# Kernel optimization log

Hardware: AMD Instinct MI355X
Metric: run time of the kernel (lower is better)

The kernel has to match this reference:

```python
import jax, jax.numpy as jnp
import numpy as np

B, N, C = 4, 4096, 16
HID, HEADS, OUT = 64, 4, 64
NEG = -1e16

def setup_inputs() -> dict:
    key = jax.random.key(0)
    ks = jax.random.split(key, 7)
    x = jax.random.normal(ks[0], (B, N, C), dtype=jnp.float32)
    # sparse-ish binary adjacency with self-loops, stored dense as in the torch module
    graph = (jax.random.randint(ks[1], (N, N), 0, 2)).astype(jnp.float32)
    graph = jnp.maximum(graph, jnp.eye(N, dtype=jnp.float32))
    # per-head Linear weights (bias=False) and the per-layer bias parameter b
    Ws = jax.random.normal(ks[2], (HEADS, C, HID), dtype=jnp.float32)   # W.weight.T per head
    bs = jax.random.normal(ks[3], (HEADS, HID), dtype=jnp.float32)
    W_out = jax.random.normal(ks[4], (HEADS * HID, OUT), dtype=jnp.float32)
    b_out = jax.random.normal(ks[5], (OUT,), dtype=jnp.float32)
    return {"x": x, "graph": graph, "Ws": Ws, "bs": bs, "W_out": W_out, "b_out": b_out}

def _gat_layer(x, graph, W, b):
    # x: [B,N,Cin], W: [Cin,D], b: [D]
    h = jnp.einsum('bnc,cd->bnd', x, W)                      # [B,N,D]
    s = jnp.einsum('bnd,bmd->bnm', h, h) * graph[None]       # [B,N,N]
    s = jnp.where(s == 0.0, NEG, s)                          # masked_fill(eq 0, -1e16)
    attn = jax.nn.softmax(s, axis=2)
    return jnp.einsum('bnm,bmd->bnd', attn, h) + b

def _leaky_relu(x):
    return jnp.where(x >= 0, x, 0.2 * x)

def reference(x, graph, Ws, bs, W_out, b_out):
    # multi-head layers, concatenated on feature dim (head-major)
    heads = jax.vmap(lambda W, b: _gat_layer(x, graph, W, b))(Ws, bs)  # [H,B,N,D]
    cat = jnp.transpose(heads, (1, 2, 0, 3)).reshape(B, N, HEADS * HID)
    cat = _leaky_relu(cat)
    out = _gat_layer(cat, graph, W_out, b_out)
    return _leaky_relu(out)
```

## Files before the change

### kernel.cpp

```cpp
#include <hip/hip_runtime.h>

typedef unsigned short u16;
typedef unsigned int u32;
typedef unsigned long long u64;
typedef __attribute__((ext_vector_type(8))) short bf16x8;
typedef __attribute__((ext_vector_type(4))) float f32x4;
typedef __attribute__((ext_vector_type(16))) float f32x16;

#define NEGF  -1.0e38f
#define MINIT -1.0e30f
#define LOG2E 1.4426950408889634f

__device__ __forceinline__ u16 f2bf(float x) {
  union { float f; u32 u; } v; v.f = x;
  u32 r = v.u + 0x7fffu + ((v.u >> 16) & 1u);
  return (u16)(r >> 16);
}
__device__ __forceinline__ float bf2f(u16 b) {
  union { u32 u; float f; } v; v.u = ((u32)b) << 16;
  return v.f;
}
__device__ __forceinline__ float bcast(u32 u) {
  union { u32 u; float f; } v; v.u = u; return v.f;
}
__device__ __forceinline__ u32 cvtpk(float a, float b) {
  u32 r;
  asm("v_cvt_pk_bf16_f32 %0, %1, %2" : "=v"(r) : "v"(a), "v"(b));
  return r;
}
__device__ __forceinline__ float vexp2(float x) {
  float r;
  asm("v_exp_f32 %0, %1" : "=v"(r) : "v"(x));
  return r;
}
__device__ __forceinline__ float fmax3(float a, float b, float c) {
  return fmaxf(fmaxf(a, b), c);
}
__device__ __forceinline__ float leaky(float x) { return x >= 0.f ? x : 0.2f * x; }

__device__ __forceinline__ void gload16(const void* g, void* l) {
  __builtin_amdgcn_global_load_lds(
      (const __attribute__((address_space(1))) u32*)(unsigned long long)g,
      (__attribute__((address_space(3))) u32*)(u32)(unsigned long long)l,
      16, 0, 0);
}

#define GRP   1040
#define TILE  8320
#define KA_OFF 0
#define KB_OFF 8320
#define KC_OFF 16640
#define V_OFF  24960
#define SMEM_BYTES 58240

__global__ __launch_bounds__(256) void pack_kernel(const float* __restrict__ graph,
                                                   u64* __restrict__ bits) {
  const int n = blockIdx.x;
  const int w = threadIdx.x >> 6, lane = threadIdx.x & 63;
  const float* gr = graph + (size_t)n * 4096;
  for (int j = 0; j < 16; ++j) {
    const int wd = j * 4 + w;
    u64 m = __ballot(gr[wd * 64 + lane] != 0.0f);
    if (lane == 0) bits[(size_t)wd * 4096 + n] = m;
  }
}

__global__ __launch_bounds__(256) void h1_kernel(const float* __restrict__ x,
                                                 const float* __restrict__ Ws,
                                                 u16* __restrict__ h1a, u16* __restrict__ h1b,
                                                 u16* __restrict__ h1c,
                                                 u16* __restrict__ h1aT, u16* __restrict__ h1bT) {
  const int n0 = blockIdx.x * 64;
  const int p  = blockIdx.y;
  const int b = p >> 2, h = p & 3;
  const int t = threadIdx.x;
  const int d = t & 63, rg = t >> 6;
  __shared__ float xt[64][17];
  __shared__ u16 ta[64][66];
  __shared__ u16 tb[64][66];
  {
    const float4 v = *(const float4*)(x + ((size_t)b * 4096 + n0 + (t >> 2)) * 16 + (t & 3) * 4);
    xt[t >> 2][(t & 3) * 4 + 0] = v.x;
    xt[t >> 2][(t & 3) * 4 + 1] = v.y;
    xt[t >> 2][(t & 3) * 4 + 2] = v.z;
    xt[t >> 2][(t & 3) * 4 + 3] = v.w;
  }
  float Wd[16];
  #pragma unroll
  for (int c = 0; c < 16; ++c) Wd[c] = Ws[h * (16 * 64) + c * 64 + d];
  __syncthreads();
  #pragma unroll
  for (int it = 0; it < 16; ++it) {
    const int r = it * 4 + rg;
    float acc = 0.f;
    #pragma unroll
    for (int c = 0; c < 16; ++c) acc += xt[r][c] * Wd[c];
    const size_t o = ((size_t)p * 4096 + n0 + r) * 64 + d;
    u16 a = f2bf(acc);
    float r1 = acc - bf2f(a);
    u16 bq = f2bf(r1);
    float r2 = r1 - bf2f(bq);
    h1a[o] = a; h1b[o] = bq; h1c[o] = f2bf(r2);
    ta[r][d] = a; tb[r][d] = bq;
  }
  __syncthreads();
  const int cs = (d & 51) | ((d & 4) << 1) | ((d & 8) >> 1);
  #pragma unroll
  for (int i = 0; i < 16; ++i) {
    const int dr = i * 4 + rg;
    h1aT[((size_t)p * 64 + dr) * 4096 + n0 + cs] = ta[d][dr];
    h1bT[((size_t)p * 64 + dr) * 4096 + n0 + cs] = tb[d][dr];
  }
}

__global__ __launch_bounds__(256) void transpose_kernel(const u16* __restrict__ src,
                                                        u16* __restrict__ dst) {
  const int p = blockIdx.y, n0 = blockIdx.x * 64;
  const u16* s = src + (size_t)p * 4096 * 64;
  u16* d = dst + (size_t)p * 4096 * 64;
  __shared__ u16 tile[64][66];
  const int col = threadIdx.x & 63, r4 = threadIdx.x >> 6;
  #pragma unroll
  for (int i = 0; i < 16; ++i) {
    const int r = i * 4 + r4;
    tile[r][col] = s[(size_t)(n0 + r) * 64 + col];
  }
  __syncthreads();
  const int cs = (col & 51) | ((col & 4) << 1) | ((col & 8) >> 1);
  #pragma unroll
  for (int i = 0; i < 16; ++i) {
    const int r = i * 4 + r4;
    d[(size_t)r * 4096 + n0 + cs] = tile[col][r];
  }
}

__global__ __launch_bounds__(256) void h2_kernel(const float* __restrict__ cat,
                                                 const float* __restrict__ Wout,
                                                 u16* __restrict__ h2a, u16* __restrict__ h2b,
                                                 u16* __restrict__ h2c) {
  const int row = blockIdx.x * 4 + (threadIdx.x >> 6);
  const int d = threadIdx.x & 63;
  const float* cr = cat + (size_t)row * 256;
  float acc = 0.f;
  for (int c4 = 0; c4 < 64; ++c4) {
    const float4 cv = *(const float4*)(cr + c4 * 4);
    acc += cv.x * Wout[(c4 * 4 + 0) * 64 + d];
    acc += cv.y * Wout[(c4 * 4 + 1) * 64 + d];
    acc += cv.z * Wout[(c4 * 4 + 2) * 64 + d];
    acc += cv.w * Wout[(c4 * 4 + 3) * 64 + d];
  }
  const size_t o = (size_t)row * 64 + d;
  u16 a = f2bf(acc);
  float r1 = acc - bf2f(a);
  u16 bq = f2bf(r1);
  float r2 = r1 - bf2f(bq);
  h2a[o] = a; h2b[o] = bq; h2c[o] = f2bf(r2);
}

template <int LAYER>
__global__ __launch_bounds__(256) void attn_kernel(
    const u16* __restrict__ Ha, const u16* __restrict__ Hb, const u16* __restrict__ Hc,
    const u16* __restrict__ HaT, const u16* __restrict__ HbT,
    const u64* __restrict__ bits, const float* __restrict__ bias,
    float* __restrict__ outp, float* __restrict__ pm, float* __restrict__ pl) {
  constexpr int NCH = (LAYER == 1) ? 64 : 16;
  const int orig = blockIdx.x + 32 * blockIdx.y;
  const int sid = (orig & 7) * 64 + (orig >> 3);
  const int bx = sid & 31;
  const int py = sid >> 5;
  const int pass = (LAYER == 1) ? py : (py & 3);
  const int chg0 = (LAYER == 1) ? 0 : ((py >> 2) * 16);

  const int t = threadIdx.x;
  const int wq = t >> 6;
  const int lane = t & 63;
  const int c = lane & 31;
  const int g1 = lane >> 5;
  const int qbase = bx * 128 + wq * 32;
  const int q = qbase + c;
  const size_t poffb = (size_t)pass * (4096 * 64) * 2;

  __shared__ f32x4 smem_v[SMEM_BYTES / 16];
  char* smem = (char*)smem_v;

  const int srow = lane >> 3;
  const int scol = ((lane & 7) ^ srow) << 4;
  const char* gKa = (const char*)Ha + poffb;
  const char* gKb = (const char*)Hb + poffb;
  const char* gKc = (const char*)Hc + poffb;
  const char* gVa = (const char*)HaT + poffb;
  const char* gVb = (const char*)HbT + poffb;

  auto stageK = [&](int chg) {
    const size_t cb = (size_t)chg * 8192;
    #pragma unroll
    for (int ii = 0; ii < 2; ++ii) {
      const int g = wq * 2 + ii;
      const size_t so = cb + (size_t)(g * 8 + srow) * 128 + scol;
      const int dofs = g * GRP;
      gload16(gKa + so, smem + KA_OFF + dofs);
      gload16(gKb + so, smem + KB_OFF + dofs);
      gload16(gKc + so, smem + KC_OFF + dofs);
    }
  };
  auto stageV = [&](int chg, int buf) {
    const char* gsrc = (wq >> 1) ? gVb : gVa;
    char* dbase = smem + V_OFF + buf * 16640 + (wq >> 1) * TILE;
    const size_t cb = (size_t)chg * 128;
    #pragma unroll
    for (int ii = 0; ii < 4; ++ii) {
      const int g = (wq & 1) * 4 + ii;
      const size_t so = cb + (size_t)(g * 8 + srow) * 8192 + scol;
      gload16(gsrc + so, dbase + g * GRP);
    }
  };

  bf16x8 qf[3][4];
  {
    const char* qra = (const char*)Ha + poffb + (size_t)q * 128 + 16 * g1;
    const char* qrb = (const char*)Hb + poffb + (size_t)q * 128 + 16 * g1;
    const char* qrc = (const char*)Hc + poffb + (size_t)q * 128 + 16 * g1;
    #pragma unroll
    for (int kk = 0; kk < 4; ++kk) {
      qf[0][kk] = *(const bf16x8*)(qra + kk * 32);
      qf[1][kk] = *(const bf16x8*)(qrb + kk * 32);
      qf[2][kk] = *(const bf16x8*)(qrc + kk * 32);
    }
  }

  const u64* bqp = bits + q;

  const int swz = (c & 7) << 4;
  int iK[4];
  #pragma unroll
  for (int kk = 0; kk < 4; ++kk)
    iK[kk] = c * 128 + ((c >> 3) << 4) + ((32 * kk + 16 * g1) ^ swz);

  const f32x16 z16 = {};
  f32x16 Of0, Of1;
  #pragma unroll
  for (int r = 0; r < 16; ++r) { Of0[r] = 0.f; Of1[r] = 0.f; }
  float mrow = MINIT, lrow = 0.f;

  stageK(chg0);
  stageV(chg0, 0);
  u64 mcur = bqp[(size_t)chg0 * 4096];
  asm volatile("s_waitcnt vmcnt(0)" ::: "memory");
  __syncthreads();

  #pragma unroll 1
  for (int ch = 0; ch < NCH; ++ch) {
    const int chg = chg0 + ch;
    __builtin_amdgcn_sched_barrier(0);
    f32x16 s0, s1;
    __builtin_amdgcn_s_setprio(1);
    #pragma unroll
    for (int kk = 0; kk < 4; ++kk) {
      const char* kp0 = smem + iK[kk];
      const char* kp1 = smem + 4 * GRP + iK[kk];
      const bf16x8 ka0 = *(const bf16x8*)(kp0 + KA_OFF);
      const bf16x8 kb0 = *(const bf16x8*)(kp0 + KB_OFF);
      const bf16x8 kc0 = *(const bf16x8*)(kp0 + KC_OFF);
      const bf16x8 ka1 = *(const bf16x8*)(kp1 + KA_OFF);
      const bf16x8 kb1 = *(const bf16x8*)(kp1 + KB_OFF);
      const bf16x8 kc1 = *(const bf16x8*)(kp1 + KC_OFF);
      s0 = __builtin_amdgcn_mfma_f32_32x32x16_bf16(ka0, qf[2][kk], kk ? s0 : z16, 0, 0, 0);
      s1 = __builtin_amdgcn_mfma_f32_32x32x16_bf16(ka1, qf[2][kk], kk ? s1 : z16, 0, 0, 0);
      s0 = __builtin_amdgcn_mfma_f32_32x32x16_bf16(kb0, qf[1][kk], s0, 0, 0, 0);
      s1 = __builtin_amdgcn_mfma_f32_32x32x16_bf16(kb1, qf[1][kk], s1, 0, 0, 0);
      s0 = __builtin_amdgcn_mfma_f32_32x32x16_bf16(kc0, qf[0][kk], s0, 0, 0, 0);
      s1 = __builtin_amdgcn_mfma_f32_32x32x16_bf16(kc1, qf[0][kk], s1, 0, 0, 0);
      s0 = __builtin_amdgcn_mfma_f32_32x32x16_bf16(ka0, qf[1][kk], s0, 0, 0, 0);
      s1 = __builtin_amdgcn_mfma_f32_32x32x16_bf16(ka1, qf[1][kk], s1, 0, 0, 0);
      s0 = __builtin_amdgcn_mfma_f32_32x32x16_bf16(kb0, qf[0][kk], s0, 0, 0, 0);
      s1 = __builtin_amdgcn_mfma_f32_32x32x16_bf16(kb1, qf[0][kk], s1, 0, 0, 0);
      s0 = __builtin_amdgcn_mfma_f32_32x32x16_bf16(ka0, qf[0][kk], s0, 0, 0, 0);
      s1 = __builtin_amdgcn_mfma_f32_32x32x16_bf16(ka1, qf[0][kk], s1, 0, 0, 0);
    }
    __builtin_amdgcn_s_setprio(0);
    __builtin_amdgcn_sched_barrier(0);
    __builtin_amdgcn_s_barrier();
    __builtin_amdgcn_sched_barrier(0);
    if (ch + 1 < NCH) {
      stageK(chg + 1);
      stageV(chg + 1, (ch + 1) & 1);
    }
    __builtin_amdgcn_sched_barrier(0);

    const u32 a0 = (u32)(mcur >> (4 * g1));
    const u32 a1 = (u32)(mcur >> (32 + 4 * g1));
    #pragma unroll
    for (int r = 0; r < 16; ++r) {
      const int off = (r & 3) + 8 * (r >> 2);
      s0[r] = ((a0 >> off) & 1u) ? s0[r] : NEGF;
      s1[r] = ((a1 >> off) & 1u) ? s1[r] : NEGF;
    }
    float t0 = fmax3(s0[0], s0[1], s0[2]);
    float t1 = fmax3(s0[3], s0[4], s0[5]);
    float t2 = fmax3(s0[6], s0[7], s0[8]);
    float t3 = fmax3(s0[9], s0[10], s0[11]);
    float t4 = fmax3(s0[12], s0[13], s0[14]);
    float t5 = fmax3(s0[15], s1[0], s1[1]);
    float t6 = fmax3(s1[2], s1[3], s1[4]);
    float t7 = fmax3(s1[5], s1[6], s1[7]);
    float t8 = fmax3(s1[8], s1[9], s1[10]);
    float t9 = fmax3(s1[11], s1[12], s1[13]);
    float ta = fmaxf(s1[14], s1[15]);
    float u0 = fmax3(t0, t1, t2);
    float u1 = fmax3(t3, t4, t5);
    float u2 = fmax3(t6, t7, t8);
    float u3 = fmax3(t9, ta, u0);
    float mm = fmax3(u1, u2, u3);
    mm = fmaxf(mm, __shfl_xor(mm, 32));
    if (!__all(mm <= mrow + 8.f)) {
      const float mn = fmaxf(mrow, mm);
      const float scl = vexp2((mrow - mn) * LOG2E);
      #pragma unroll
      for (int r = 0; r < 16; ++r) { Of0[r] *= scl; Of1[r] *= scl; }
      lrow *= scl;
      mrow = mn;
    }
    if (LAYER == 1) {
      const float mL = mrow * LOG2E;
      #pragma unroll
      for (int r = 0; r < 16; ++r) {
        s0[r] = vexp2(__builtin_fmaf(s0[r], LOG2E, -mL));
        s1[r] = vexp2(__builtin_fmaf(s1[r], LOG2E, -mL));
      }
    } else {
      #pragma unroll
      for (int r = 0; r < 16; ++r) {
        s0[r] = vexp2((s0[r] - mrow) * LOG2E);
        s1[r] = vexp2((s1[r] - mrow) * LOG2E);
      }
    }
    {
      float r4[4];
      #pragma unroll
      for (int j = 0; j < 4; ++j)
        r4[j] = ((s0[4*j] + s0[4*j+1]) + (s0[4*j+2] + s0[4*j+3]))
              + ((s1[4*j] + s1[4*j+1]) + (s1[4*j+2] + s1[4*j+3]));
      float rs = (r4[0] + r4[1]) + (r4[2] + r4[3]);
      rs += __shfl_xor(rs, 32);
      lrow += rs;
    }

    bf16x8 pa[4], pb[4];
    #pragma unroll
    for (int kk = 0; kk < 4; ++kk) {
      const f32x16& sm = (kk >> 1) ? s1 : s0;
      const int rb = 8 * (kk & 1);
      union { u32 w[4]; bf16x8 v; } ua, ub;
      #pragma unroll
      for (int j = 0; j < 4; ++j) {
        const float p0 = sm[rb + 2*j], p1 = sm[rb + 2*j + 1];
        const u32 h = cvtpk(p0, p1);
        ua.w[j] = h;
        const float h0f = bcast(h << 16);
        const float h1f = bcast(h & 0xffff0000u);
        ub.w[j] = cvtpk(p0 - h0f, p1 - h1f);
      }
      pa[kk] = ua.v; pb[kk] = ub.v;
    }

    const char* vbase = smem + V_OFF + (ch & 1) * 16640;
    __builtin_amdgcn_s_setprio(1);
    #pragma unroll
    for (int kk = 0; kk < 4; ++kk) {
      const char* vp0 = vbase + iK[kk];
      const char* vp1 = vbase + 4 * GRP + iK[kk];
      const bf16x8 va0 = *(const bf16x8*)(vp0);
      const bf16x8 vb0 = *(const bf16x8*)(vp0 + TILE);
      const bf16x8 va1 = *(const bf16x8*)(vp1);
      const bf16x8 vb1 = *(const bf16x8*)(vp1 + TILE);
      Of0 = __builtin_amdgcn_mfma_f32_32x32x16_bf16(vb0, pa[kk], Of0, 0, 0, 0);
      Of1 = __builtin_amdgcn_mfma_f32_32x32x16_bf16(vb1, pa[kk], Of1, 0, 0, 0);
      Of0 = __builtin_amdgcn_mfma_f32_32x32x16_bf16(va0, pb[kk], Of0, 0, 0, 0);
      Of1 = __builtin_amdgcn_mfma_f32_32x32x16_bf16(va1, pb[kk], Of1, 0, 0, 0);
      Of0 = __builtin_amdgcn_mfma_f32_32x32x16_bf16(va0, pa[kk], Of0, 0, 0, 0);
      Of1 = __builtin_amdgcn_mfma_f32_32x32x16_bf16(va1, pa[kk], Of1, 0, 0, 0);
    }
    __builtin_amdgcn_s_setprio(0);

    u64 mnxt = 0;
    if (ch + 1 < NCH) mnxt = bqp[(size_t)(chg + 1) * 4096];
    __builtin_amdgcn_sched_barrier(0);
    if (ch + 1 < NCH) {
      asm volatile("s_waitcnt vmcnt(1)" ::: "memory");
    } else {
      asm volatile("s_waitcnt vmcnt(0)" ::: "memory");
    }
    __builtin_amdgcn_sched_barrier(0);
    __builtin_amdgcn_s_barrier();
    mcur = mnxt;
  }

  char* reg = smem + wq * 8704;
  const float inv = (LAYER == 1) ? (1.0f / lrow) : 1.0f;
  #pragma unroll
  for (int dt = 0; dt < 2; ++dt) {
    const f32x16& o = dt ? Of1 : Of0;
    #pragma unroll
    for (int i = 0; i < 4; ++i) {
      f32x4 v;
      v[0] = o[4*i+0] * inv; v[1] = o[4*i+1] * inv;
      v[2] = o[4*i+2] * inv; v[3] = o[4*i+3] * inv;
      *(f32x4*)(reg + c * 272 + (32 * dt + 8 * i + 4 * g1) * 4) = v;
    }
  }
  if (LAYER == 2 && lane < 32) {
    pm[(size_t)py * 4096 + q] = mrow;
    pl[(size_t)py * 4096 + q] = lrow;
  }
  __syncthreads();
  const int d0 = (lane & 15) * 4;
  const float* bp = (LAYER == 1) ? (bias + (pass & 3) * 64) : bias;
  #pragma unroll
  for (int qq = 0; qq < 8; ++qq) {
    const int ql = qq * 4 + (lane >> 4);
    f32x4 v = *(const f32x4*)(reg + ql * 272 + (lane & 15) * 16);
    const int qg = qbase + ql;
    if (LAYER == 1) {
      v[0] = leaky(v[0] + bp[d0 + 0]);
      v[1] = leaky(v[1] + bp[d0 + 1]);
      v[2] = leaky(v[2] + bp[d0 + 2]);
      v[3] = leaky(v[3] + bp[d0 + 3]);
      *(f32x4*)&outp[((size_t)((pass >> 2) * 4096 + qg)) * 256 + (pass & 3) * 64 + d0] = v;
    } else {
      *(f32x4*)&outp[((size_t)py * 4096 + qg) * 64 + d0] = v;
    }
  }
}

__global__ __launch_bounds__(256) void merge_kernel(
    const float* __restrict__ pO, const float* __restrict__ pm, const float* __restrict__ pl,
    const float* __restrict__ bo, float* __restrict__ dout) {
  const int t = threadIdx.x;
  const int d = t & 63;
  const int q = blockIdx.x * 4 + (t >> 6);
  const int pass = blockIdx.y;
  float m[4], l[4], o[4];
  #pragma unroll
  for (int s = 0; s < 4; ++s) {
    const size_t idx = (size_t)(s * 4 + pass) * 4096 + q;
    m[s] = pm[idx]; l[s] = pl[idx];
    o[s] = pO[idx * 64 + d];
  }
  const float M = fmaxf(fmaxf(m[0], m[1]), fmaxf(m[2], m[3]));
  float num = 0.f, den = 0.f;
  #pragma unroll
  for (int s = 0; s < 4; ++s) {
    const float w = exp2f((m[s] - M) * LOG2E);
    num += w * o[s]; den += w * l[s];
  }
  const float r = num / den + bo[d];
  dout[((size_t)pass * 4096 + q) * 64 + d] = leaky(r);
}

extern "C" void kernel_launch(void* const* d_in, const int* in_sizes, int n_in,
                              void* d_out, int out_size, void* d_ws, size_t ws_size,
                              hipStream_t stream) {
  const float* x     = (const float*)d_in[0];
  const float* graph = (const float*)d_in[1];
  const float* Ws    = (const float*)d_in[2];
  const float* bs    = (const float*)d_in[3];
  const float* W_out = (const float*)d_in[4];
  const float* b_out = (const float*)d_in[5];
  char* ws = (char*)d_ws;
  const size_t MiB = 1048576;

  u64* bits   = (u64*)(ws + 0 * MiB);
  u16* h1a    = (u16*)(ws + 2 * MiB);
  u16* h1b    = (u16*)(ws + 10 * MiB);
  u16* h1c    = (u16*)(ws + 18 * MiB);
  u16* h1aT   = (u16*)(ws + 26 * MiB);
  u16* h1bT   = (u16*)(ws + 34 * MiB);
  float* catb = (float*)(ws + 42 * MiB);
  u16* h2a    = (u16*)(ws + 58 * MiB);
  u16* h2b    = (u16*)(ws + 60 * MiB);
  u16* h2c    = (u16*)(ws + 62 * MiB);
  u16* h2aT   = (u16*)(ws + 64 * MiB);
  u16* h2bT   = (u16*)(ws + 66 * MiB);
  float* pO   = (float*)(ws + 2 * MiB);
  float* pmb  = (float*)(ws + 18 * MiB);
  float* plb  = (float*)(ws + 18 * MiB + 262144);

  pack_kernel<<<4096, 256, 0, stream>>>(graph, bits);
  h1_kernel<<<dim3(64, 16), 256, 0, stream>>>(x, Ws, h1a, h1b, h1c, h1aT, h1bT);
  attn_kernel<1><<<dim3(32, 16), 256, 0, stream>>>(h1a, h1b, h1c, h1aT, h1bT,
                                                   bits, bs, catb, nullptr, nullptr);
  h2_kernel<<<4096, 256, 0, stream>>>(catb, W_out, h2a, h2b, h2c);
  transpose_kernel<<<dim3(64, 4), 256, 0, stream>>>(h2a, h2aT);
  transpose_kernel<<<dim3(64, 4), 256, 0, stream>>>(h2b, h2bT);
  attn_kernel<2><<<dim3(32, 16), 256, 0, stream>>>(h2a, h2b, h2c, h2aT, h2bT,
                                                   bits, b_out, pO, pmb, plb);
  merge_kernel<<<dim3(1024, 4), 256, 0, stream>>>(pO, pmb, plb, b_out, (float*)d_out);
}
```

Baseline: 436.6 us.

## Software-pipeline next chunk's QK^T MFMAs with current chunk's softmax

Restructures the attention loop so the score MFMAs for chunk ch+1 are split into two halves and interleaved with the masking, max, exp and bf16 split of chunk ch. It uses two ping-pong score register sets, and the loop is manually unrolled by two. K staging is moved one chunk further ahead, and the V and mask loads are moved before the PV MFMAs. The aim is to hide the VALU softmax work behind matrix-core work. The cost is higher register pressure from the extra accumulators, and the loop appears to assume an even chunk count.

```diff
diff --git a/kernel.cpp b/kernel.cpp
--- a/kernel.cpp
+++ b/kernel.cpp
@@ -241,71 +241,77 @@
   #pragma unroll
   for (int r = 0; r < 16; ++r) { Of0[r] = 0.f; Of1[r] = 0.f; }
   float mrow = MINIT, lrow = 0.f;
-
-  stageK(chg0);
-  stageV(chg0, 0);
-  u64 mcur = bqp[(size_t)chg0 * 4096];
+  u64 mcur;
+  bf16x8 pa[4], pb[4];
+
+  auto Sstep = [&](f32x16& n0, f32x16& n1, int kk) {
+    const char* kp0 = smem + iK[kk];
+    const char* kp1 = smem + 4 * GRP + iK[kk];
+    const bf16x8 ka0 = *(const bf16x8*)(kp0 + KA_OFF);
+    const bf16x8 kb0 = *(const bf16x8*)(kp0 + KB_OFF);
+    const bf16x8 kc0 = *(const bf16x8*)(kp0 + KC_OFF);
+    const bf16x8 ka1 = *(const bf16x8*)(kp1 + KA_OFF);
+    const bf16x8 kb1 = *(const bf16x8*)(kp1 + KB_OFF);
+    const bf16x8 kc1 = *(const bf16x8*)(kp1 + KC_OFF);
+    n0 = __builtin_amdgcn_mfma_f32_32x32x16_bf16(ka0, qf[2][kk], kk ? n0 : z16, 0, 0, 0);
+    n1 = __builtin_amdgcn_mfma_f32_32x32x16_bf16(ka1, qf[2][kk], kk ? n1 : z16, 0, 0, 0);
+    n0 = __builtin_amdgcn_mfma_f32_32x32x16_bf16(kb0, qf[1][kk], n0, 0, 0, 0);
+    n1 = __builtin_amdgcn_mfma_f32_32x32x16_bf16(kb1, qf[1][kk], n1, 0, 0, 0);
+    n0 = __builtin_amdgcn_mfma_f32_32x32x16_bf16(kc0, qf[0][kk], n0, 0, 0, 0);
+    n1 = __builtin_amdgcn_mfma_f32_32x32x16_bf16(kc1, qf[0][kk], n1, 0, 0, 0);
+    n0 = __builtin_amdgcn_mfma_f32_32x32x16_bf16(ka0, qf[1][kk], n0, 0, 0, 0);
+    n1 = __builtin_amdgcn_mfma_f32_32x32x16_bf16(ka1, qf[1][kk], n1, 0, 0, 0);
+    n0 = __builtin_amdgcn_mfma_f32_32x32x16_bf16(kb0, qf[0][kk], n0, 0, 0, 0);
+    n1 = __builtin_amdgcn_mfma_f32_32x32x16_bf16(kb1, qf[0][kk], n1, 0, 0, 0);
+    n0 = __builtin_amdgcn_mfma_f32_32x32x16_bf16(ka0, qf[0][kk], n0, 0, 0, 0);
+    n1 = __builtin_amdgcn_mfma_f32_32x32x16_bf16(ka1, qf[0][kk], n1, 0, 0, 0);
+  };
+
+  f32x16 sA0, sA1, sB0, sB1;
+
+  stageK(chg0); stageV(chg0, 0);
+  __builtin_amdgcn_sched_barrier(0);
+  mcur = bqp[(size_t)chg0 * 4096];
+  __builtin_amdgcn_sched_barrier(0);
   asm volatile("s_waitcnt vmcnt(0)" ::: "memory");
   __syncthreads();
-
-  #pragma unroll 1
-  for (int ch = 0; ch < NCH; ++ch) {
+  __builtin_amdgcn_s_setprio(1);
+  Sstep(sA0, sA1, 0); Sstep(sA0, sA1, 1); Sstep(sA0, sA1, 2); Sstep(sA0, sA1, 3);
+  __builtin_amdgcn_s_setprio(0);
+  __builtin_amdgcn_sched_barrier(0);
+  __builtin_amdgcn_s_barrier();
+  __builtin_amdgcn_sched_barrier(0);
+  if (NCH > 1) stageK(chg0 + 1);
+  __builtin_amdgcn_sched_barrier(0);
+  asm volatile("s_waitcnt vmcnt(0)" ::: "memory");
+  __builtin_amdgcn_sched_barrier(0);
+  __builtin_amdgcn_s_barrier();
+
+  auto iterbody = [&](int ch, f32x16& c0, f32x16& c1, f32x16& n0, f32x16& n1) {
     const int chg = chg0 + ch;
-    __builtin_amdgcn_sched_barrier(0);
-    f32x16 s0, s1;
+    const bool hasNext = (ch + 1 < NCH);
     __builtin_amdgcn_s_setprio(1);
-    #pragma unroll
-    for (int kk = 0; kk < 4; ++kk) {
-      const char* kp0 = smem + iK[kk];
-      const char* kp1 = smem + 4 * GRP + iK[kk];
-      const bf16x8 ka0 = *(const bf16x8*)(kp0 + KA_OFF);
-      const bf16x8 kb0 = *(const bf16x8*)(kp0 + KB_OFF);
-      const bf16x8 kc0 = *(const bf16x8*)(kp0 + KC_OFF);
-      const bf16x8 ka1 = *(const bf16x8*)(kp1 + KA_OFF);
-      const bf16x8 kb1 = *(const bf16x8*)(kp1 + KB_OFF);
-      const bf16x8 kc1 = *(const bf16x8*)(kp1 + KC_OFF);
-      s0 = __builtin_amdgcn_mfma_f32_32x32x16_bf16(ka0, qf[2][kk], kk ? s0 : z16, 0, 0, 0);
-      s1 = __builtin_amdgcn_mfma_f32_32x32x16_bf16(ka1, qf[2][kk], kk ? s1 : z16, 0, 0, 0);
-      s0 = __builtin_amdgcn_mfma_f32_32x32x16_bf16(kb0, qf[1][kk], s0, 0, 0, 0);
-      s1 = __builtin_amdgcn_mfma_f32_32x32x16_bf16(kb1, qf[1][kk], s1, 0, 0, 0);
-      s0 = __builtin_amdgcn_mfma_f32_32x32x16_bf16(kc0, qf[0][kk], s0, 0, 0, 0);
-      s1 = __builtin_amdgcn_mfma_f32_32x32x16_bf16(kc1, qf[0][kk], s1, 0, 0, 0);
-      s0 = __builtin_amdgcn_mfma_f32_32x32x16_bf16(ka0, qf[1][kk], s0, 0, 0, 0);
-      s1 = __builtin_amdgcn_mfma_f32_32x32x16_bf16(ka1, qf[1][kk], s1, 0, 0, 0);
-      s0 = __builtin_amdgcn_mfma_f32_32x32x16_bf16(kb0, qf[0][kk], s0, 0, 0, 0);
-      s1 = __builtin_amdgcn_mfma_f32_32x32x16_bf16(kb1, qf[0][kk], s1, 0, 0, 0);
-      s0 = __builtin_amdgcn_mfma_f32_32x32x16_bf16(ka0, qf[0][kk], s0, 0, 0, 0);
-      s1 = __builtin_amdgcn_mfma_f32_32x32x16_bf16(ka1, qf[0][kk], s1, 0, 0, 0);
-    }
+    if (hasNext) { Sstep(n0, n1, 0); Sstep(n0, n1, 1); }
     __builtin_amdgcn_s_setprio(0);
-    __builtin_amdgcn_sched_barrier(0);
-    __builtin_amdgcn_s_barrier();
-    __builtin_amdgcn_sched_barrier(0);
-    if (ch + 1 < NCH) {
-      stageK(chg + 1);
-      stageV(chg + 1, (ch + 1) & 1);
-    }
-    __builtin_amdgcn_sched_barrier(0);
-
     const u32 a0 = (u32)(mcur >> (4 * g1));
     const u32 a1 = (u32)(mcur >> (32 + 4 * g1));
     #pragma unroll
     for (int r = 0; r < 16; ++r) {
       const int off = (r & 3) + 8 * (r >> 2);
-      s0[r] = ((a0 >> off) & 1u) ? s0[r] : NEGF;
-      s1[r] = ((a1 >> off) & 1u) ? s1[r] : NEGF;
-    }
-    float t0 = fmax3(s0[0], s0[1], s0[2]);
-    float t1 = fmax3(s0[3], s0[4], s0[5]);
-    float t2 = fmax3(s0[6], s0[7], s0[8]);
-    float t3 = fmax3(s0[9], s0[10], s0[11]);
-    float t4 = fmax3(s0[12], s0[13], s0[14]);
-    float t5 = fmax3(s0[15], s1[0], s1[1]);
-    float t6 = fmax3(s1[2], s1[3], s1[4]);
-    float t7 = fmax3(s1[5], s1[6], s1[7]);
-    float t8 = fmax3(s1[8], s1[9], s1[10]);
-    float t9 = fmax3(s1[11], s1[12], s1[13]);
-    float ta = fmaxf(s1[14], s1[15]);
+      c0[r] = ((a0 >> off) & 1u) ? c0[r] : NEGF;
+      c1[r] = ((a1 >> off) & 1u) ? c1[r] : NEGF;
+    }
+    float t0 = fmax3(c0[0], c0[1], c0[2]);
+    float t1 = fmax3(c0[3], c0[4], c0[5]);
+    float t2 = fmax3(c0[6], c0[7], c0[8]);
+    float t3 = fmax3(c0[9], c0[10], c0[11]);
+    float t4 = fmax3(c0[12], c0[13], c0[14]);
+    float t5 = fmax3(c0[15], c1[0], c1[1]);
+    float t6 = fmax3(c1[2], c1[3], c1[4]);
+    float t7 = fmax3(c1[5], c1[6], c1[7]);
+    float t8 = fmax3(c1[8], c1[9], c1[10]);
+    float t9 = fmax3(c1[11], c1[12], c1[13]);
+    float ta = fmaxf(c1[14], c1[15]);
     float u0 = fmax3(t0, t1, t2);
     float u1 = fmax3(t3, t4, t5);
     float u2 = fmax3(t6, t7, t8);
@@ -320,35 +326,36 @@
       lrow *= scl;
       mrow = mn;
     }
+    __builtin_amdgcn_s_setprio(1);
+    if (hasNext) { Sstep(n0, n1, 2); Sstep(n0, n1, 3); }
+    __builtin_amdgcn_s_setprio(0);
     if (LAYER == 1) {
       const float mL = mrow * LOG2E;
       #pragma unroll
       for (int r = 0; r < 16; ++r) {
-        s0[r] = vexp2(__builtin_fmaf(s0[r], LOG2E, -mL));
-        s1[r] = vexp2(__builtin_fmaf(s1[r], LOG2E, -mL));
+        c0[r] = vexp2(__builtin_fmaf(c0[r], LOG2E, -mL));
+        c1[r] = vexp2(__builtin_fmaf(c1[r], LOG2E, -mL));
       }
     } else {
       #pragma unroll
       for (int r = 0; r < 16; ++r) {
-        s0[r] = vexp2((s0[r] - mrow) * LOG2E);
-        s1[r] = vexp2((s1[r] - mrow) * LOG2E);
+        c0[r] = vexp2((c0[r] - mrow) * LOG2E);
+        c1[r] = vexp2((c1[r] - mrow) * LOG2E);
       }
     }
     {
       float r4[4];
       #pragma unroll
       for (int j = 0; j < 4; ++j)
-        r4[j] = ((s0[4*j] + s0[4*j+1]) + (s0[4*j+2] + s0[4*j+3]))
-              + ((s1[4*j] + s1[4*j+1]) + (s1[4*j+2] + s1[4*j+3]));
+        r4[j] = ((c0[4*j] + c0[4*j+1]) + (c0[4*j+2] + c0[4*j+3]))
+              + ((c1[4*j] + c1[4*j+1]) + (c1[4*j+2] + c1[4*j+3]));
       float rs = (r4[0] + r4[1]) + (r4[2] + r4[3]);
       rs += __shfl_xor(rs, 32);
       lrow += rs;
     }
-
-    bf16x8 pa[4], pb[4];
     #pragma unroll
     for (int kk = 0; kk < 4; ++kk) {
-      const f32x16& sm = (kk >> 1) ? s1 : s0;
+      const f32x16& sm = (kk >> 1) ? c1 : c0;
       const int rb = 8 * (kk & 1);
       union { u32 w[4]; bf16x8 v; } ua, ub;
       #pragma unroll
@@ -356,13 +363,18 @@
         const float p0 = sm[rb + 2*j], p1 = sm[rb + 2*j + 1];
         const u32 h = cvtpk(p0, p1);
         ua.w[j] = h;
-        const float h0f = bcast(h << 16);
-        const float h1f = bcast(h & 0xffff0000u);
-        ub.w[j] = cvtpk(p0 - h0f, p1 - h1f);
+        ub.w[j] = cvtpk(p0 - bcast(h << 16), p1 - bcast(h & 0xffff0000u));
       }
       pa[kk] = ua.v; pb[kk] = ub.v;
     }
-
+    __builtin_amdgcn_sched_barrier(0);
+    __builtin_amdgcn_s_barrier();
+    __builtin_amdgcn_sched_barrier(0);
+    if (ch + 2 < NCH) stageK(chg + 2);
+    if (hasNext) stageV(chg + 1, (ch + 1) & 1);
+    __builtin_amdgcn_sched_barrier(0);
+    if (hasNext) mcur = bqp[(size_t)(chg + 1) * 4096];
+    __builtin_amdgcn_sched_barrier(0);
     const char* vbase = smem + V_OFF + (ch & 1) * 16640;
     __builtin_amdgcn_s_setprio(1);
     #pragma unroll
@@ -381,18 +393,20 @@
       Of1 = __builtin_amdgcn_mfma_f32_32x32x16_bf16(va1, pa[kk], Of1, 0, 0, 0);
     }
     __builtin_amdgcn_s_setprio(0);
-
-    u64 mnxt = 0;
-    if (ch + 1 < NCH) mnxt = bqp[(size_t)(chg + 1) * 4096];
     __builtin_amdgcn_sched_barrier(0);
-    if (ch + 1 < NCH) {
+    if (hasNext) {
       asm volatile("s_waitcnt vmcnt(1)" ::: "memory");
     } else {
       asm volatile("s_waitcnt vmcnt(0)" ::: "memory");
     }
     __builtin_amdgcn_sched_barrier(0);
     __builtin_amdgcn_s_barrier();
-    mcur = mnxt;
+  };
+
+  #pragma unroll 1
+  for (int ch2 = 0; ch2 < NCH; ch2 += 2) {
+    iterbody(ch2, sA0, sA1, sB0, sB1);
+    iterbody(ch2 + 1, sB0, sB1, sA0, sA1);
   }
 
   char* reg = smem + wq * 8704;
```

Result: slower. 541.5 us (+24.0%).
